# Performance work log

Measured on AMD Instinct MI355X. Metric: run time of the kernel, lower is better.

Reference implementation:

```python
import jax, jax.numpy as jnp
import numpy as np

N = 50000
E = 800000
F_IN = 128
HEADS = 8
HID = 16
CLASSES = 40
NEG_SLOPE = 0.2


def setup_inputs() -> dict:
    key = jax.random.key(0)
    ks = jax.random.split(key, 10)
    return {
        "x": jax.random.normal(ks[0], (N, F_IN), jnp.float32),
        "edge_index": jax.random.randint(ks[1], (2, E), 0, N, jnp.int64),
        "W1": jax.random.normal(ks[2], (F_IN, HEADS * HID), jnp.float32) * 0.1,
        "a_src1": jax.random.normal(ks[3], (HEADS, HID), jnp.float32) * 0.1,
        "a_dst1": jax.random.normal(ks[4], (HEADS, HID), jnp.float32) * 0.1,
        "b1": jax.random.normal(ks[5], (HEADS * HID,), jnp.float32) * 0.1,
        "W2": jax.random.normal(ks[6], (HEADS * HID, CLASSES), jnp.float32) * 0.1,
        "a_src2": jax.random.normal(ks[7], (1, CLASSES), jnp.float32) * 0.1,
        "a_dst2": jax.random.normal(ks[8], (1, CLASSES), jnp.float32) * 0.1,
        "b2": jax.random.normal(ks[9], (CLASSES,), jnp.float32) * 0.1,
    }


def gat_conv(x, src, dst, W, a_src, a_dst, bias, heads, out_ch, concat):
    # x: [N, in] -> h: [N, H, C]
    h = (x @ W).reshape(N, heads, out_ch)
    e_src = jnp.einsum("nhc,hc->nh", h, a_src)  # [N, H]
    e_dst = jnp.einsum("nhc,hc->nh", h, a_dst)
    alpha = e_src[src] + e_dst[dst]             # [E, H]
    alpha = jax.nn.leaky_relu(alpha, NEG_SLOPE)
    # segment softmax over incoming edges of each dst node
    amax = jax.ops.segment_max(alpha, dst, num_segments=N)
    alpha = jnp.exp(alpha - amax[dst])
    denom = jax.ops.segment_sum(alpha, dst, num_segments=N)
    alpha = alpha / (denom[dst] + 1e-16)
    msg = h[src] * alpha[:, :, None]            # [E, H, C]
    out = jax.ops.segment_sum(msg, dst, num_segments=N)  # [N, H, C]
    out = out.reshape(N, heads * out_ch) if concat else out.mean(axis=1)
    return out + bias


def reference(x, edge_index, W1, a_src1, a_dst1, b1, W2, a_src2, a_dst2, b2):
    # PyG GATConv adds self-loops by default
    loops = jnp.arange(N, dtype=edge_index.dtype)
    src = jnp.concatenate([edge_index[0], loops])
    dst = jnp.concatenate([edge_index[1], loops])
    # inference: dropout layers are identity
    h = gat_conv(x, src, dst, W1, a_src1, a_dst1, b1, HEADS, HID, concat=True)
    h = jax.nn.elu(h)
    out = gat_conv(h, src, dst, W2, a_src2, a_dst2, b2, 1, CLASSES, concat=False)
    return out
```

## Files before the change

kernel.cpp:

```cpp
#include <hip/hip_runtime.h>
#include <math.h>

#define NN 50000
#define EE 800000
#define ET (EE + NN)
#define F_IN 128
#define HEADS 8
#define HID 16
#define C1 (HEADS * HID)
#define CLASSES 40
#define NEG_SLOPE 0.2f
#define LOG2E 1.4426950408889634f

#define NCHUNKS ((NN + 1023) / 1024)
#define NHIST 64
#define EPB (EE / NHIST)
#define PADN (NCHUNKS * 1024)
#define LDSW (PADN / 4)
#define GB ((NN + 63) / 64)

typedef __attribute__((ext_vector_type(8))) short bf16x8;
typedef __attribute__((ext_vector_type(4))) float f32x4;
typedef __attribute__((ext_vector_type(8))) _Float16 h16x8;
typedef __attribute__((ext_vector_type(2))) _Float16 h16x2;

__device__ __forceinline__ unsigned cvtpk(float a, float b) {
    unsigned r;
    asm("v_cvt_pk_bf16_f32 %0, %1, %2" : "=v"(r) : "v"(a), "v"(b));
    return r;
}
__device__ __forceinline__ float fexp2(float x) {
    float r;
    asm("v_exp_f32 %0, %1\n\ts_nop 0" : "=v"(r) : "v"(x));
    return r;
}
__device__ __forceinline__ float bflo(unsigned u) { return __uint_as_float(u << 16); }
__device__ __forceinline__ float bfhi(unsigned u) { return __uint_as_float(u & 0xffff0000u); }
__device__ __forceinline__ float lrelu(float a) { return fmaxf(a, NEG_SLOPE * a); }
__device__ __forceinline__ unsigned short bf1(float a) { return (unsigned short)cvtpk(a, a); }
__device__ __forceinline__ float bf1f(float a) { return bflo(cvtpk(a, a)); }
__device__ __forceinline__ bf16x8 pack8(float f0, float f1, float f2, float f3,
                                        float f4, float f5, float f6, float f7) {
    union { unsigned u[4]; bf16x8 v; } U;
    U.u[0] = cvtpk(f0, f1);
    U.u[1] = cvtpk(f2, f3);
    U.u[2] = cvtpk(f4, f5);
    U.u[3] = cvtpk(f6, f7);
    return U.v;
}

__global__ void prep_kernel(const float* __restrict__ W1,
                            const float* __restrict__ as1, const float* __restrict__ ad1,
                            const float* __restrict__ W2,
                            const float* __restrict__ as2, const float* __restrict__ ad2,
                            const int* __restrict__ ei,
                            unsigned short* __restrict__ va1h, unsigned short* __restrict__ va1l,
                            unsigned short* __restrict__ va2b,
                            unsigned short* __restrict__ W1b, unsigned short* __restrict__ W2b,
                            unsigned char* __restrict__ partial8) {
    const int tid = threadIdx.x;
    const int b = blockIdx.x;
    if (b >= 3) {
        __shared__ unsigned lhist[LDSW];
        for (int i = tid; i < LDSW; i += 256) lhist[i] = 0;
        __syncthreads();
        const int hb = b - 3;
        const int* dp = ei + EE + hb * EPB;
        for (int e0 = tid * 4; e0 < EPB; e0 += 1024) {
            int4 d4 = *(const int4*)(dp + e0);
            atomicAdd(&lhist[(unsigned)d4.x >> 2], 1u << (((unsigned)d4.x & 3) << 3));
            atomicAdd(&lhist[(unsigned)d4.y >> 2], 1u << (((unsigned)d4.y & 3) << 3));
            atomicAdd(&lhist[(unsigned)d4.z >> 2], 1u << (((unsigned)d4.z & 3) << 3));
            atomicAdd(&lhist[(unsigned)d4.w >> 2], 1u << (((unsigned)d4.w & 3) << 3));
        }
        __syncthreads();
        unsigned* pb = (unsigned*)(partial8 + (size_t)hb * PADN);
        for (int i = tid; i < LDSW; i += 256) pb[i] = lhist[i];
        return;
    }
    if (b == 1) {
        for (int f = tid; f < 2048; f += 256) {
            const int lane = f & 63, kc = (f >> 6) & 3, ntw = f >> 8;
            const int q = lane >> 4, c = lane & 15;
            const int col = ntw * 16 + c;
            const int k0 = kc * 32 + q * 8;
            const float* wp = W1 + (size_t)k0 * C1 + col;
            *(bf16x8*)(W1b + (size_t)f * 8) =
                pack8(wp[0], wp[C1], wp[2 * C1], wp[3 * C1],
                      wp[4 * C1], wp[5 * C1], wp[6 * C1], wp[7 * C1]);
        }
        return;
    }
    if (b == 2) {
        for (int f = tid; f < 768; f += 256) {
            const int lane = f & 63, kc = (f >> 6) & 3, nt = f >> 8;
            const int q = lane >> 4, c = lane & 15;
            const int col = nt * 16 + c;
            const int k0 = kc * 32 + q * 8;
            bf16x8 v = 0;
            if (col < CLASSES) {
                const float* wp = W2 + (size_t)k0 * CLASSES + col;
                v = pack8(wp[0], wp[CLASSES], wp[2 * CLASSES], wp[3 * CLASSES],
                          wp[4 * CLASSES], wp[5 * CLASSES], wp[6 * CLASSES], wp[7 * CLASSES]);
            }
            *(bf16x8*)(W2b + (size_t)f * 8) = v;
        }
        return;
    }
    {
        const int k = tid >> 1, half = tid & 1;
        const float* wrow = W1 + (size_t)k * C1 + half * 64;
        #pragma unroll
        for (int hh = 0; hh < 4; ++hh) {
            const int h = half * 4 + hh;
            float s = 0.f, d = 0.f;
            #pragma unroll
            for (int t = 0; t < 16; ++t) {
                float wv = wrow[hh * 16 + t];
                s += wv * as1[h * HID + t];
                d += wv * ad1[h * HID + t];
            }
            s *= LOG2E; d *= LOG2E;
            va1h[h * 128 + k]       = bf1(s);
            va1l[h * 128 + k]       = bf1(s - bf1f(s));
            va1h[(h + 8) * 128 + k] = bf1(d);
            va1l[(h + 8) * 128 + k] = bf1(d - bf1f(d));
        }
    }
    if (tid < C1) {
        const float* wrow = W2 + (size_t)tid * CLASSES;
        float s = 0.f, d = 0.f;
        #pragma unroll
        for (int c2 = 0; c2 < CLASSES; ++c2) {
            float wv = wrow[c2];
            s += wv * as2[c2];
            d += wv * ad2[c2];
        }
        s *= LOG2E; d *= LOG2E;
        va2b[0 * 128 + tid] = bf1(s);
        va2b[1 * 128 + tid] = bf1(s - bf1f(s));
        va2b[2 * 128 + tid] = bf1(d);
        va2b[3 * 128 + tid] = bf1(d - bf1f(d));
    }
}

__global__ void scan1_kernel(const unsigned char* __restrict__ partial8,
                             unsigned char* __restrict__ pfx8,
                             int* __restrict__ deg,
                             int* __restrict__ rowptr, int* __restrict__ bsum) {
    __shared__ int sh[256];
    const int tid = threadIdx.x;
    const int base = blockIdx.x * 1024 + tid * 4;
    int t0 = 0, t1 = 0, t2 = 0, t3 = 0;
    #pragma unroll 8
    for (int b = 0; b < NHIST; ++b) {
        uchar4 pf;
        pf.x = (unsigned char)t0; pf.y = (unsigned char)t1;
        pf.z = (unsigned char)t2; pf.w = (unsigned char)t3;
        *(uchar4*)(pfx8 + (size_t)b * PADN + base) = pf;
        uchar4 p = *(const uchar4*)(partial8 + (size_t)b * PADN + base);
        t0 += p.x; t1 += p.y; t2 += p.z; t3 += p.w;
    }
    int v[4], s[4];
    v[0] = (base + 0 < NN) ? t0 + 1 : 0;
    v[1] = (base + 1 < NN) ? t1 + 1 : 0;
    v[2] = (base + 2 < NN) ? t2 + 1 : 0;
    v[3] = (base + 3 < NN) ? t3 + 1 : 0;
    #pragma unroll
    for (int j = 0; j < 4; ++j)
        if (base + j < NN) deg[base + j] = v[j];
    s[0] = v[0]; s[1] = s[0] + v[1]; s[2] = s[1] + v[2]; s[3] = s[2] + v[3];
    int T = s[3];
    sh[tid] = T;
    __syncthreads();
    for (int off = 1; off < 256; off <<= 1) {
        int xv = (tid >= off) ? sh[tid - off] : 0;
        __syncthreads();
        sh[tid] += xv;
        __syncthreads();
    }
    int excl = sh[tid] - T;
    #pragma unroll
    for (int j = 0; j < 4; ++j)
        if (base + j < NN) rowptr[base + j] = excl + s[j] - v[j];
    if (tid == 255) bsum[blockIdx.x] = sh[255];
}

__global__ void scan3_kernel(int* __restrict__ rowptr, const int* __restrict__ bsum,
                             unsigned short* __restrict__ csr) {
    __shared__ int ex[64];
    const int tid = threadIdx.x;
    if (tid < 64) {
        int v = (tid < NCHUNKS) ? bsum[tid] : 0;
        int s = v;
        #pragma unroll
        for (int off = 1; off < 64; off <<= 1) {
            int xv = __shfl_up(s, off);
            if (tid >= off) s += xv;
        }
        ex[tid] = s - v;
    }
    __syncthreads();
    int i = blockIdx.x * blockDim.x + tid;
    if (i >= NN) return;
    int rp = rowptr[i] + ex[i >> 10];
    rowptr[i] = rp;
    csr[rp] = (unsigned short)i;
}

__global__ __launch_bounds__(256, 3)
void gemm1_fill_kernel(const float* __restrict__ x,
                       const unsigned short* __restrict__ W1b,
                       const unsigned short* __restrict__ va1h,
                       const unsigned short* __restrict__ va1l,
                       const int* __restrict__ ei,
                       const int* __restrict__ rowptr,
                       const unsigned char* __restrict__ pfx8,
                       unsigned short* __restrict__ csr,
                       _Float16* __restrict__ h1h,
                       float* __restrict__ e_src, float* __restrict__ e_dst) {
    const int bid = blockIdx.x;
    const int tid = threadIdx.x;
    __shared__ unsigned lrank[LDSW];
    if (bid < NHIST) {
        for (int i = tid; i < LDSW; i += 256) lrank[i] = 0;
        __syncthreads();
        const int fb = bid;
        const int* sp = ei + fb * EPB;
        const int* dp = ei + EE + fb * EPB;
        const unsigned char* pf = pfx8 + (size_t)fb * PADN;
        for (int e0 = tid * 4; e0 < EPB; e0 += 1024) {
            int4 s4 = *(const int4*)(sp + e0);
            int4 d4 = *(const int4*)(dp + e0);
            {
                const unsigned d = (unsigned)d4.x, sh8 = (d & 3) << 3;
                unsigned old = atomicAdd(&lrank[d >> 2], 1u << sh8);
                csr[rowptr[d] + 1 + pf[d] + ((old >> sh8) & 0xff)] = (unsigned short)s4.x;
            }
            {
                const unsigned d = (unsigned)d4.y, sh8 = (d & 3) << 3;
                unsigned old = atomicAdd(&lrank[d >> 2], 1u << sh8);
                csr[rowptr[d] + 1 + pf[d] + ((old >> sh8) & 0xff)] = (unsigned short)s4.y;
            }
            {
                const unsigned d = (unsigned)d4.z, sh8 = (d & 3) << 3;
                unsigned old = atomicAdd(&lrank[d >> 2], 1u << sh8);
                csr[rowptr[d] + 1 + pf[d] + ((old >> sh8) & 0xff)] = (unsigned short)s4.z;
            }
            {
                const unsigned d = (unsigned)d4.w, sh8 = (d & 3) << 3;
                unsigned old = atomicAdd(&lrank[d >> 2], 1u << sh8);
                csr[rowptr[d] + 1 + pf[d] + ((old >> sh8) & 0xff)] = (unsigned short)s4.w;
            }
        }
        return;
    }
    const int gemmb = bid - NHIST;
    const int w = tid >> 6, lane = tid & 63;
    const int q = lane >> 4, c = lane & 15;
    const int m0 = (gemmb * 4 + w) * 16;

    int row = m0 + c;
    if (row > NN - 1) row = NN - 1;
    bf16x8 afrag[4];
    #pragma unroll
    for (int kc = 0; kc < 4; ++kc) {
        const float* xp = x + (size_t)row * F_IN + kc * 32 + q * 8;
        float4 p0 = *(const float4*)xp;
        float4 p1 = *(const float4*)(xp + 4);
        afrag[kc] = pack8(p0.x, p0.y, p0.z, p0.w, p1.x, p1.y, p1.z, p1.w);
    }

    {
        f32x4 acce = {0.f, 0.f, 0.f, 0.f};
        #pragma unroll
        for (int kc = 0; kc < 4; ++kc) {
            const int coloff = kc * 32 + q * 8;
            bf16x8 beh = *(const bf16x8*)(va1h + c * 128 + coloff);
            bf16x8 bel = *(const bf16x8*)(va1l + c * 128 + coloff);
            acce = __builtin_amdgcn_mfma_f32_16x16x32_bf16(afrag[kc], beh, acce, 0, 0, 0);
            acce = __builtin_amdgcn_mfma_f32_16x16x32_bf16(afrag[kc], bel, acce, 0, 0, 0);
        }
        float* ep = (c < 8) ? e_src : e_dst;
        const int cc = c & 7;
        #pragma unroll
        for (int r = 0; r < 4; ++r) {
            const int ro = m0 + q * 4 + r;
            if (ro < NN) ep[(size_t)ro * HEADS + cc] = acce[r];
        }
    }

    #pragma unroll 2
    for (int nt = 0; nt < 8; ++nt) {
        bf16x8 bf0 = *(const bf16x8*)(W1b + (size_t)((nt * 4 + 0) * 64 + lane) * 8);
        bf16x8 bf1_ = *(const bf16x8*)(W1b + (size_t)((nt * 4 + 1) * 64 + lane) * 8);
        bf16x8 bf2 = *(const bf16x8*)(W1b + (size_t)((nt * 4 + 2) * 64 + lane) * 8);
        bf16x8 bf3 = *(const bf16x8*)(W1b + (size_t)((nt * 4 + 3) * 64 + lane) * 8);
        f32x4 a = {0.f, 0.f, 0.f, 0.f};
        a = __builtin_amdgcn_mfma_f32_16x16x32_bf16(afrag[0], bf0, a, 0, 0, 0);
        a = __builtin_amdgcn_mfma_f32_16x16x32_bf16(afrag[1], bf1_, a, 0, 0, 0);
        a = __builtin_amdgcn_mfma_f32_16x16x32_bf16(afrag[2], bf2, a, 0, 0, 0);
        a = __builtin_amdgcn_mfma_f32_16x16x32_bf16(afrag[3], bf3, a, 0, 0, 0);
        #pragma unroll
        for (int r = 0; r < 4; ++r) {
            const int ro = m0 + q * 4 + r;
            if (ro < NN) h1h[(size_t)ro * C1 + nt * 16 + c] = (_Float16)a[r];
        }
    }
}

__global__ __launch_bounds__(64)
void agg1_kernel(const _Float16* __restrict__ h1h,
                 const float* __restrict__ e_src, const float* __restrict__ e_dst,
                 const int* __restrict__ rowptr, const int* __restrict__ deg,
                 const unsigned short* __restrict__ csr,
                 const float* __restrict__ b1, unsigned short* __restrict__ hmid) {
    const int tid = threadIdx.x;
    const int l = tid & 15;
    const int d = blockIdx.x * 4 + (tid >> 4);
    const int hd = l >> 1;
    const float ed = e_dst[(size_t)d * HEADS + hd];
    const int start = rowptr[d];
    const int cnt = deg[d];

    float denom = 0.f;
    float acc[8] = {0.f, 0.f, 0.f, 0.f, 0.f, 0.f, 0.f, 0.f};

    for (int i = 0; i < cnt; i += 8) {
        int s[8];
        #pragma unroll
        for (int e = 0; e < 8; ++e)
            s[e] = csr[start + ((i + e < cnt) ? i + e : i)];
        float es[8];
        #pragma unroll
        for (int e = 0; e < 8; ++e)
            es[e] = e_src[(size_t)s[e] * HEADS + hd];
        h16x8 g[8];
        #pragma unroll
        for (int e = 0; e < 8; ++e)
            g[e] = *(const h16x8*)(h1h + (size_t)s[e] * C1 + 8 * l);
        float w[8];
        #pragma unroll
        for (int e = 0; e < 8; ++e) {
            float we = fexp2(lrelu(es[e] + ed));
            w[e] = (i + e < cnt) ? we : 0.f;
            denom += w[e];
        }
        #pragma unroll
        for (int e = 0; e < 8; ++e) {
            #pragma unroll
            for (int j = 0; j < 8; ++j)
                acc[j] = fmaf((float)g[e][j], w[e], acc[j]);
        }
    }
    const float inv = 1.f / (denom + 1e-16f);
    float o[8];
    #pragma unroll
    for (int k = 0; k < 8; ++k) {
        float t = acc[k] * inv + b1[8 * l + k];
        o[k] = (t > 0.f) ? t : fexp2(t * LOG2E) - 1.f;
    }
    uint4 st;
    st.x = cvtpk(o[0], o[1]);
    st.y = cvtpk(o[2], o[3]);
    st.z = cvtpk(o[4], o[5]);
    st.w = cvtpk(o[6], o[7]);
    *(uint4*)(hmid + (size_t)d * C1 + 8 * l) = st;
}

__global__ __launch_bounds__(256, 4)
void gemm2_kernel(const unsigned short* __restrict__ hmid,
                  const unsigned short* __restrict__ W2b,
                  const unsigned short* __restrict__ va2b,
                  _Float16* __restrict__ h2h,
                  float* __restrict__ e_src, float* __restrict__ e_dst) {
    const int tid = threadIdx.x;
    const int w = tid >> 6, lane = tid & 63;
    const int q = lane >> 4, c = lane & 15;

    const int m0 = (blockIdx.x * 4 + w) * 16;
    if (m0 >= NN) return;
    int row = m0 + c;
    if (row > NN - 1) row = NN - 1;
    bf16x8 afrag[4];
    #pragma unroll
    for (int kc = 0; kc < 4; ++kc)
        afrag[kc] = *(const bf16x8*)(hmid + (size_t)row * C1 + kc * 32 + q * 8);

    bf16x8 bfrag[3][4];
    #pragma unroll
    for (int nt = 0; nt < 3; ++nt)
        #pragma unroll
        for (int kc = 0; kc < 4; ++kc)
            bfrag[nt][kc] = *(const bf16x8*)(W2b + (size_t)((nt * 4 + kc) * 64 + lane) * 8);
    bf16x8 bfe[4];
    #pragma unroll
    for (int kc = 0; kc < 4; ++kc) {
        bf16x8 bb = 0;
        if (c < 4) bb = *(const bf16x8*)(va2b + c * 128 + kc * 32 + q * 8);
        bfe[kc] = bb;
    }

    f32x4 acc[3] = {{0.f,0.f,0.f,0.f},{0.f,0.f,0.f,0.f},{0.f,0.f,0.f,0.f}};
    f32x4 acce = {0.f, 0.f, 0.f, 0.f};
    #pragma unroll
    for (int kc = 0; kc < 4; ++kc) {
        acc[0] = __builtin_amdgcn_mfma_f32_16x16x32_bf16(afrag[kc], bfrag[0][kc], acc[0], 0, 0, 0);
        acc[1] = __builtin_amdgcn_mfma_f32_16x16x32_bf16(afrag[kc], bfrag[1][kc], acc[1], 0, 0, 0);
        acc[2] = __builtin_amdgcn_mfma_f32_16x16x32_bf16(afrag[kc], bfrag[2][kc], acc[2], 0, 0, 0);
        acce   = __builtin_amdgcn_mfma_f32_16x16x32_bf16(afrag[kc], bfe[kc],      acce,   0, 0, 0);
    }
    #pragma unroll
    for (int r = 0; r < 4; ++r) {
        const int ro = m0 + q * 4 + r;
        float v = acce[r] + __shfl_xor(acce[r], 1);
        if (ro < NN) {
            #pragma unroll
            for (int nt = 0; nt < 3; ++nt) {
                const int col = nt * 16 + c;
                if (col < CLASSES)
                    h2h[(size_t)ro * CLASSES + col] = (_Float16)acc[nt][r];
            }
            if (c == 0) e_src[ro] = v;
            if (c == 2) e_dst[ro] = v;
        }
    }
}

__global__ __launch_bounds__(64)
void agg2_kernel(const _Float16* __restrict__ h2h,
                 const float* __restrict__ e_src, const float* __restrict__ e_dst,
                 const int* __restrict__ rowptr, const int* __restrict__ deg,
                 const unsigned short* __restrict__ csr,
                 const float* __restrict__ b2, float* __restrict__ out) {
    const int tid = threadIdx.x;
    const int eg = tid / 20;
    const int c  = tid % 20;
    const int d = blockIdx.x * 3 + eg;
    const bool live = (eg < 3) && (d < NN);
    const int dcl = live ? d : 0;
    const float ed = e_dst[dcl];
    const int start = rowptr[dcl];
    const int cnt = live ? deg[dcl] : 0;

    float denom = 0.f, acc0 = 0.f, acc1 = 0.f;
    for (int i = 0; i < cnt; i += 8) {
        int s[8];
        #pragma unroll
        for (int e = 0; e < 8; ++e)
            s[e] = csr[start + ((i + e < cnt) ? i + e : i)];
        float es[8];
        #pragma unroll
        for (int e = 0; e < 8; ++e)
            es[e] = e_src[s[e]];
        h16x2 g[8];
        #pragma unroll
        for (int e = 0; e < 8; ++e)
            g[e] = *(const h16x2*)(h2h + (size_t)s[e] * CLASSES + 2 * c);
        float w[8];
        #pragma unroll
        for (int e = 0; e < 8; ++e) {
            float we = fexp2(lrelu(es[e] + ed));
            w[e] = (i + e < cnt) ? we : 0.f;
            denom += w[e];
        }
        #pragma unroll
        for (int e = 0; e < 8; ++e) {
            acc0 = fmaf((float)g[e][0], w[e], acc0);
            acc1 = fmaf((float)g[e][1], w[e], acc1);
        }
    }
    if (live) {
        const float inv = 1.f / (denom + 1e-16f);
        float2 o;
        o.x = acc0 * inv + b2[2 * c];
        o.y = acc1 * inv + b2[2 * c + 1];
        *(float2*)(out + (size_t)d * CLASSES + 2 * c) = o;
    }
}

extern "C" void kernel_launch(void* const* d_in, const int* in_sizes, int n_in,
                              void* d_out, int out_size, void* d_ws, size_t ws_size,
                              hipStream_t stream) {
    const float* x      = (const float*)d_in[0];
    const int*   ei     = (const int*)d_in[1];
    const float* W1     = (const float*)d_in[2];
    const float* a_src1 = (const float*)d_in[3];
    const float* a_dst1 = (const float*)d_in[4];
    const float* b1     = (const float*)d_in[5];
    const float* W2     = (const float*)d_in[6];
    const float* a_src2 = (const float*)d_in[7];
    const float* a_dst2 = (const float*)d_in[8];
    const float* b2     = (const float*)d_in[9];
    float* out = (float*)d_out;

    char* ws = (char*)d_ws;
    size_t off = 0;
    auto alloc = [&](size_t bytes) { char* p = ws + off; off += (bytes + 255) & ~(size_t)255; return p; };
    _Float16* h1h = (_Float16*)alloc((size_t)NN * C1 * 2);
    _Float16* h2h = (_Float16*)alloc((size_t)NN * CLASSES * 2);
    unsigned short* hmidb = (unsigned short*)alloc((size_t)NN * C1 * 2);
    float* e_src1 = (float*)alloc((size_t)NN * HEADS * 4);
    float* e_dst1 = (float*)alloc((size_t)NN * HEADS * 4);
    float* e_src2 = (float*)alloc((size_t)NN * 4);
    float* e_dst2 = (float*)alloc((size_t)NN * 4);
    int*   deg    = (int*)alloc((size_t)NN * 4);
    int*   rowptr = (int*)alloc((size_t)NN * 4);
    unsigned short* csr  = (unsigned short*)alloc((size_t)ET * 2);
    int*   bsum   = (int*)alloc(256 * 4);
    unsigned short* va1h = (unsigned short*)alloc(16 * 128 * 2);
    unsigned short* va1l = (unsigned short*)alloc(16 * 128 * 2);
    unsigned short* va2b = (unsigned short*)alloc(4 * 128 * 2);
    unsigned short* W1b  = (unsigned short*)alloc(2048 * 8 * 2);
    unsigned short* W2b  = (unsigned short*)alloc(768 * 8 * 2);
    unsigned char* partial8 = (unsigned char*)alloc((size_t)NHIST * PADN);
    unsigned char* pfx8     = (unsigned char*)alloc((size_t)NHIST * PADN);

    prep_kernel<<<3 + NHIST, 256, 0, stream>>>(W1, a_src1, a_dst1, W2, a_src2, a_dst2, ei,
                                               va1h, va1l, va2b, W1b, W2b, partial8);
    scan1_kernel<<<NCHUNKS, 256, 0, stream>>>(partial8, pfx8, deg, rowptr, bsum);
    scan3_kernel<<<(NN + 255) / 256, 256, 0, stream>>>(rowptr, bsum, csr);
    gemm1_fill_kernel<<<NHIST + GB, 256, 0, stream>>>(x, W1b, va1h, va1l, ei, rowptr, pfx8,
                                                      csr, h1h, e_src1, e_dst1);

    agg1_kernel<<<NN / 4, 64, 0, stream>>>(h1h, e_src1, e_dst1, rowptr, deg, csr, b1, hmidb);

    gemm2_kernel<<<(NN + 63) / 64, 256, 0, stream>>>(hmidb, W2b, va2b, h2h, e_src2, e_dst2);
    agg2_kernel<<<(NN + 2) / 3, 64, 0, stream>>>(h2h, e_src2, e_dst2, rowptr, deg, csr, b2, out);
}
```

Before: 206.1 us.

## Record per-edge ranks during histogram pass and drop LDS atomics in CSR fill

The histogram pass in prep_kernel now stores each edge's local rank, the old value returned by its LDS atomic, into a new byte array. The CSR fill blocks in gemm1_fill then read this rank instead of repeating the LDS atomic counting. That removes their ~50KB shared array, so gemm1_fill's launch bounds are raised to allow 4 blocks per CU. The cost is an extra 800KB write and read of rank bytes.

```diff
diff --git a/kernel.cpp b/kernel.cpp
--- a/kernel.cpp
+++ b/kernel.cpp
@@ -57,7 +57,8 @@
                             unsigned short* __restrict__ va1h, unsigned short* __restrict__ va1l,
                             unsigned short* __restrict__ va2b,
                             unsigned short* __restrict__ W1b, unsigned short* __restrict__ W2b,
-                            unsigned char* __restrict__ partial8) {
+                            unsigned char* __restrict__ partial8,
+                            unsigned char* __restrict__ rank8) {
     const int tid = threadIdx.x;
     const int b = blockIdx.x;
     if (b >= 3) {
@@ -66,12 +67,31 @@
         __syncthreads();
         const int hb = b - 3;
         const int* dp = ei + EE + hb * EPB;
+        unsigned char* rk = rank8 + (size_t)hb * EPB;
         for (int e0 = tid * 4; e0 < EPB; e0 += 1024) {
             int4 d4 = *(const int4*)(dp + e0);
-            atomicAdd(&lhist[(unsigned)d4.x >> 2], 1u << (((unsigned)d4.x & 3) << 3));
-            atomicAdd(&lhist[(unsigned)d4.y >> 2], 1u << (((unsigned)d4.y & 3) << 3));
-            atomicAdd(&lhist[(unsigned)d4.z >> 2], 1u << (((unsigned)d4.z & 3) << 3));
-            atomicAdd(&lhist[(unsigned)d4.w >> 2], 1u << (((unsigned)d4.w & 3) << 3));
+            uchar4 r;
+            {
+                const unsigned d = (unsigned)d4.x, sh8 = (d & 3) << 3;
+                unsigned old = atomicAdd(&lhist[d >> 2], 1u << sh8);
+                r.x = (unsigned char)((old >> sh8) & 0xff);
+            }
+            {
+                const unsigned d = (unsigned)d4.y, sh8 = (d & 3) << 3;
+                unsigned old = atomicAdd(&lhist[d >> 2], 1u << sh8);
+                r.y = (unsigned char)((old >> sh8) & 0xff);
+            }
+            {
+                const unsigned d = (unsigned)d4.z, sh8 = (d & 3) << 3;
+                unsigned old = atomicAdd(&lhist[d >> 2], 1u << sh8);
+                r.z = (unsigned char)((old >> sh8) & 0xff);
+            }
+            {
+                const unsigned d = (unsigned)d4.w, sh8 = (d & 3) << 3;
+                unsigned old = atomicAdd(&lhist[d >> 2], 1u << sh8);
+                r.w = (unsigned char)((old >> sh8) & 0xff);
+            }
+            *(uchar4*)(rk + e0) = r;
         }
         __syncthreads();
         unsigned* pb = (unsigned*)(partial8 + (size_t)hb * PADN);
@@ -208,7 +228,7 @@
     csr[rp] = (unsigned short)i;
 }
 
-__global__ __launch_bounds__(256, 3)
+__global__ __launch_bounds__(256, 4)
 void gemm1_fill_kernel(const float* __restrict__ x,
                        const unsigned short* __restrict__ W1b,
                        const unsigned short* __restrict__ va1h,
@@ -216,42 +236,26 @@
                        const int* __restrict__ ei,
                        const int* __restrict__ rowptr,
                        const unsigned char* __restrict__ pfx8,
+                       const unsigned char* __restrict__ rank8,
                        unsigned short* __restrict__ csr,
                        _Float16* __restrict__ h1h,
                        float* __restrict__ e_src, float* __restrict__ e_dst) {
     const int bid = blockIdx.x;
     const int tid = threadIdx.x;
-    __shared__ unsigned lrank[LDSW];
     if (bid < NHIST) {
-        for (int i = tid; i < LDSW; i += 256) lrank[i] = 0;
-        __syncthreads();
         const int fb = bid;
         const int* sp = ei + fb * EPB;
         const int* dp = ei + EE + fb * EPB;
         const unsigned char* pf = pfx8 + (size_t)fb * PADN;
+        const unsigned char* rk = rank8 + (size_t)fb * EPB;
         for (int e0 = tid * 4; e0 < EPB; e0 += 1024) {
             int4 s4 = *(const int4*)(sp + e0);
             int4 d4 = *(const int4*)(dp + e0);
-            {
-                const unsigned d = (unsigned)d4.x, sh8 = (d & 3) << 3;
-                unsigned old = atomicAdd(&lrank[d >> 2], 1u << sh8);
-                csr[rowptr[d] + 1 + pf[d] + ((old >> sh8) & 0xff)] = (unsigned short)s4.x;
-            }
-            {
-                const unsigned d = (unsigned)d4.y, sh8 = (d & 3) << 3;
-                unsigned old = atomicAdd(&lrank[d >> 2], 1u << sh8);
-                csr[rowptr[d] + 1 + pf[d] + ((old >> sh8) & 0xff)] = (unsigned short)s4.y;
-            }
-            {
-                const unsigned d = (unsigned)d4.z, sh8 = (d & 3) << 3;
-                unsigned old = atomicAdd(&lrank[d >> 2], 1u << sh8);
-                csr[rowptr[d] + 1 + pf[d] + ((old >> sh8) & 0xff)] = (unsigned short)s4.z;
-            }
-            {
-                const unsigned d = (unsigned)d4.w, sh8 = (d & 3) << 3;
-                unsigned old = atomicAdd(&lrank[d >> 2], 1u << sh8);
-                csr[rowptr[d] + 1 + pf[d] + ((old >> sh8) & 0xff)] = (unsigned short)s4.w;
-            }
+            uchar4 r = *(const uchar4*)(rk + e0);
+            csr[rowptr[d4.x] + 1 + pf[d4.x] + r.x] = (unsigned short)s4.x;
+            csr[rowptr[d4.y] + 1 + pf[d4.y] + r.y] = (unsigned short)s4.y;
+            csr[rowptr[d4.z] + 1 + pf[d4.z] + r.z] = (unsigned short)s4.z;
+            csr[rowptr[d4.w] + 1 + pf[d4.w] + r.w] = (unsigned short)s4.w;
         }
         return;
     }
@@ -515,13 +519,14 @@
     unsigned short* W2b  = (unsigned short*)alloc(768 * 8 * 2);
     unsigned char* partial8 = (unsigned char*)alloc((size_t)NHIST * PADN);
     unsigned char* pfx8     = (unsigned char*)alloc((size_t)NHIST * PADN);
+    unsigned char* rank8    = (unsigned char*)alloc((size_t)EE);
 
     prep_kernel<<<3 + NHIST, 256, 0, stream>>>(W1, a_src1, a_dst1, W2, a_src2, a_dst2, ei,
-                                               va1h, va1l, va2b, W1b, W2b, partial8);
+                                               va1h, va1l, va2b, W1b, W2b, partial8, rank8);
     scan1_kernel<<<NCHUNKS, 256, 0, stream>>>(partial8, pfx8, deg, rowptr, bsum);
     scan3_kernel<<<(NN + 255) / 256, 256, 0, stream>>>(rowptr, bsum, csr);
     gemm1_fill_kernel<<<NHIST + GB, 256, 0, stream>>>(x, W1b, va1h, va1l, ei, rowptr, pfx8,
-                                                      csr, h1h, e_src1, e_dst1);
+                                                      rank8, csr, h1h, e_src1, e_dst1);
 
     agg1_kernel<<<NN / 4, 64, 0, stream>>>(h1h, e_src1, e_dst1, rowptr, deg, csr, b1, hmidb);
 
```

Result: no change. 206.4 us (+0.2%).
